# Kernel optimization log

Measured on AMD Instinct MI355X. Metric: run time of the kernel, lower is better.

Reference implementation:

```python
import jax, jax.numpy as jnp
import numpy as np
import math

H, KV, D, HID, WIN = 8, 4, 256, 2048, 1024  # heads, kv heads, head_dim, hidden, sliding window
B, S = 1, 2048

def _rms(x, scale):
    # Gemma3RMSNorm: hardcoded 1e-6 eps, (1+scale) gain
    var = jnp.mean(jnp.square(x), axis=-1, keepdims=True)
    return x * jax.lax.rsqrt(var + 1e-6) * (1.0 + scale)

def _rot_half(x):
    x1, x2 = jnp.split(x, 2, axis=-1)
    return jnp.concatenate((-x2, x1), axis=-1)

def setup_inputs() -> dict:
    key = jax.random.key(0)
    ks = jax.random.split(key, 8)
    x = jax.random.normal(ks[0], (B, S, HID), jnp.float32)
    attn_mask = jnp.ones((B, S), jnp.bool_)
    segment_pos = jnp.broadcast_to(jnp.arange(S, dtype=jnp.int32)[None], (B, S))
    # true RoPE tables, theta=1e6 (Gemma3 global layers)
    inv_freq = 1.0 / (1e6 ** (np.arange(0, D, 2, dtype=np.float32) / D))
    ang = np.arange(S, dtype=np.float32)[:, None] * inv_freq[None, :]  # [S, D/2]
    emb = np.concatenate([ang, ang], axis=-1)                          # [S, D]
    cos = jnp.asarray(np.cos(emb), jnp.float32)[None]                  # [1, S, D]
    sin = jnp.asarray(np.sin(emb), jnp.float32)[None]
    sd = 1.0 / math.sqrt(HID)
    wq = jax.random.normal(ks[1], (HID, H * D), jnp.float32) * sd
    wk = jax.random.normal(ks[2], (HID, KV * D), jnp.float32) * sd
    wv = jax.random.normal(ks[3], (HID, KV * D), jnp.float32) * sd
    wo = jax.random.normal(ks[4], (H * D, HID), jnp.float32) * (1.0 / math.sqrt(H * D))
    q_scale = jnp.zeros((D,), jnp.float32)  # zeros_init as in module
    k_scale = jnp.zeros((D,), jnp.float32)
    return dict(x=x, attn_mask=attn_mask, segment_pos=segment_pos, cos=cos, sin=sin,
                wq=wq, wk=wk, wv=wv, wo=wo, q_scale=q_scale, k_scale=k_scale)

def reference(x, attn_mask, segment_pos, cos, sin, wq, wk, wv, wo, q_scale, k_scale):
    b, s, _ = x.shape
    # projections -> [b, h, s, d]
    q = (x @ wq).reshape(b, s, H, D).transpose(0, 2, 1, 3)
    k = (x @ wk).reshape(b, s, KV, D).transpose(0, 2, 1, 3)
    v = (x @ wv).reshape(b, s, KV, D).transpose(0, 2, 1, 3)
    # per-head QK RMSNorm
    q = _rms(q, q_scale)
    k = _rms(k, k_scale)
    # RoPE (cos/sin broadcast over head axis, unsqueeze_dim=1)
    c, sn = cos[:, None], sin[:, None]
    q = q * c + _rot_half(q) * sn
    k = k * c + _rot_half(k) * sn
    # GQA: repeat-interleave kv heads
    rep = H // KV
    k = jnp.repeat(k, rep, axis=1)
    v = jnp.repeat(v, rep, axis=1)
    scores = jnp.einsum('bhqd,bhkd->bhqk', q, k) / math.sqrt(D)
    # causal + padding mask (q_len > 1 path, no image bidirectional mask)
    causal = jnp.tril(jnp.ones((s, s), jnp.bool_))
    mask = causal[None] & attn_mask[:, None, :]          # [b, q, kv]
    # sliding window mask (prefill: cache positions = arange)
    kvpos = jnp.arange(s)
    pos = segment_pos[:, :, None]
    sliding = (kvpos[None, None] > pos - WIN) & (kvpos[None, None] < pos + WIN)
    full = mask & sliding
    scores = scores + jnp.where(full[:, None], 0.0, -1e37)
    w = jax.nn.softmax(scores.astype(jnp.float32), axis=-1).astype(scores.dtype)
    out = jnp.einsum('bhqk,bhkd->bhqd', w, v)
    out = out.transpose(0, 2, 1, 3).reshape(b, s, H * D)
    return out @ wo
```

## Files before the change

kernel.cpp:

```cpp
#include <hip/hip_runtime.h>
#include <hip/hip_bf16.h>

#define S_LEN 2048
#define HID 2048
#define NH 8
#define NKV 4
#define HD 256
#define WIN 1024

typedef __hip_bfloat16 bf16;
typedef __attribute__((ext_vector_type(8))) short bf16x8;
typedef __attribute__((ext_vector_type(4))) float f32x4;

__device__ __forceinline__ void gld_lds16(void* lds, const void* g) {
    __builtin_amdgcn_global_load_lds(
        (const __attribute__((address_space(1))) unsigned int*)g,
        (__attribute__((address_space(3))) unsigned int*)lds,
        16, 0, 0);
}


__device__ __forceinline__ void transT_body(const float* __restrict__ src, bf16* __restrict__ dst,
                                            int R, int C, int r0, int c0) {
    __shared__ bf16 Ts[64][72];
    const int tid = threadIdx.x;
    {
        const int r = tid >> 2;
        const int cq = (tid & 3) * 16;
#pragma unroll
        for (int j = 0; j < 16; j += 4) {
            float4 v = *(const float4*)&src[(size_t)(r0 + r) * C + c0 + cq + j];
            Ts[cq + j + 0][r] = __float2bfloat16(v.x);
            Ts[cq + j + 1][r] = __float2bfloat16(v.y);
            Ts[cq + j + 2][r] = __float2bfloat16(v.z);
            Ts[cq + j + 3][r] = __float2bfloat16(v.w);
        }
    }
    __syncthreads();
    {
        const int c = tid >> 2;
        const int rq = (tid & 3) * 16;
#pragma unroll
        for (int j = 0; j < 16; j += 8)
            *(uint4*)&dst[(size_t)(c0 + c) * R + r0 + rq + j] = *(const uint4*)&Ts[c][rq + j];
    }
}

__global__ __launch_bounds__(256)
void prep_all(const float* __restrict__ xf, const float* __restrict__ wqf,
              const float* __restrict__ wkf, const float* __restrict__ wvf,
              const float* __restrict__ wof,
              bf16* __restrict__ xb, bf16* __restrict__ wqkvt, bf16* __restrict__ wot) {
    const int bid = blockIdx.x;
    if (bid < 2048) {
        const int i = bid * 256 + threadIdx.x;
        float4 a = ((const float4*)xf)[i * 2];
        float4 b = ((const float4*)xf)[i * 2 + 1];
        union { uint4 v; bf16 h[8]; } u;
        u.h[0] = __float2bfloat16(a.x); u.h[1] = __float2bfloat16(a.y);
        u.h[2] = __float2bfloat16(a.z); u.h[3] = __float2bfloat16(a.w);
        u.h[4] = __float2bfloat16(b.x); u.h[5] = __float2bfloat16(b.y);
        u.h[6] = __float2bfloat16(b.z); u.h[7] = __float2bfloat16(b.w);
        ((uint4*)xb)[i] = u.v;
    } else if (bid < 4096) {
        const int t = bid - 2048;
        const int bx = t & 63, by = t >> 6;
        const float* src; int C, c0, drow0;
        if (bx < 32)      { src = wqf; C = 2048; c0 = bx * 64;        drow0 = bx * 64; }
        else if (bx < 48) { src = wkf; C = 1024; c0 = (bx - 32) * 64; drow0 = 2048 + (bx - 32) * 64; }
        else              { src = wvf; C = 1024; c0 = (bx - 48) * 64; drow0 = 3072 + (bx - 48) * 64; }
        bf16* dshift = wqkvt + ((size_t)drow0 - c0) * HID;
        transT_body(src, dshift, HID, C, by * 64, c0);
    } else {
        const int t = bid - 4096;
        const int bx = t & 31, by = t >> 5;
        transT_body(wof, wot, NH * HD, HID, by * 64, bx * 64);
    }
}

template<int MODE>
__global__ __launch_bounds__(512, 2)
void gemm8p(const bf16* __restrict__ A, const bf16* __restrict__ Bt,
            bf16* __restrict__ Cb,
            bf16* __restrict__ Qo, bf16* __restrict__ Ko, bf16* __restrict__ Vto) {
    extern __shared__ bf16 smem[];
    bf16* AsP = smem;
    bf16* BsP = smem + 3 * 256 * 64;

    const int tid = threadIdx.x;
    const int w = tid >> 6, lane = tid & 63;
    const int lnm = lane & 15, quad = lane >> 4;
    const int wr = w >> 1, wc = w & 1;
    const int r8 = lane >> 3;
    const int swz = ((lane & 7) ^ r8) * 8;

    const int bid = blockIdx.x;
    const int xcd = bid & 7, idx = bid >> 3;
    int m0, n0, kbeg, nt;
    size_t zoff = 0;
    if constexpr (MODE == 1) {
        const int m_t = (xcd >> 2) * 4 + (idx >> 3);
        const int n_t = (xcd & 3) * 8 + (idx & 7);
        m0 = m_t * 256; n0 = n_t * 128; kbeg = 0; nt = 2048 / 64;
    } else {
        const int z   = xcd >> 2;
        const int n_t = (xcd & 3) * 4 + (idx & 3);
        const int m_t = idx >> 2;
        m0 = m_t * 256; n0 = n_t * 128; kbeg = z * 1024; nt = 1024 / 64;
        zoff = (size_t)z * 2048 * 2048;
    }
    const int K = 2048;

    const bf16* pA[4];
#pragma unroll
    for (int g = 0; g < 4; ++g)
        pA[g] = A + (size_t)(m0 + w * 32 + g * 8 + r8) * K + kbeg + swz;
    const bf16* pB[2];
#pragma unroll
    for (int g = 0; g < 2; ++g)
        pB[g] = Bt + (size_t)(n0 + w * 16 + g * 8 + r8) * K + kbeg + swz;
    const int dA = w * 32 * 64;
    const int dB = w * 16 * 64;

#define STG_A(slot, g, t) gld_lds16(AsP + (slot) * 16384 + dA + (g) * 512, pA[g] + (t) * 64)
#define STG_B(slot, g, t) gld_lds16(BsP + (slot) * 8192  + dB + (g) * 512, pB[g] + (t) * 64)
#define LDFRAG(base, row, kh) \
    (*(const bf16x8*)((base) + (row) * 64 + (((((kh) << 2) | quad) ^ ((row) & 7)) << 3)))

    f32x4 acc[4][4];
#pragma unroll
    for (int i = 0; i < 4; ++i)
#pragma unroll
        for (int j = 0; j < 4; ++j) acc[i][j] = (f32x4){0.f, 0.f, 0.f, 0.f};

    STG_A(0, 0, 0); STG_A(0, 1, 0); STG_A(0, 2, 0); STG_A(0, 3, 0);
    STG_B(0, 0, 0); STG_B(0, 1, 0);
    STG_A(1, 0, 1); STG_A(1, 1, 1); STG_A(1, 2, 1); STG_A(1, 3, 1);
    STG_B(1, 0, 1); STG_B(1, 1, 1);
    asm volatile("s_waitcnt vmcnt(6)" ::: "memory");
    __builtin_amdgcn_sched_barrier(0);
    __builtin_amdgcn_s_barrier();

    int sc = 0;
    for (int t = 0; t < nt; ++t) {
        const int ss = (sc == 0) ? 2 : sc - 1;
        const bf16* As_ = AsP + sc * 16384;
        const bf16* Bs_ = BsP + sc * 8192;
        const bool pf = (t + 2 < nt);

        bf16x8 a0[2][2], b[4][2];
#pragma unroll
        for (int tm = 0; tm < 2; ++tm)
#pragma unroll
            for (int kh = 0; kh < 2; ++kh)
                a0[tm][kh] = LDFRAG(As_, wr * 64 + tm * 16 + lnm, kh);
#pragma unroll
        for (int tn = 0; tn < 4; ++tn)
#pragma unroll
            for (int kh = 0; kh < 2; ++kh)
                b[tn][kh] = LDFRAG(Bs_, wc * 64 + tn * 16 + lnm, kh);
        if (pf) { STG_A(ss, 0, t + 2); STG_A(ss, 1, t + 2); STG_B(ss, 0, t + 2); }
        __builtin_amdgcn_s_barrier();
        asm volatile("s_waitcnt lgkmcnt(0)" ::: "memory");
        __builtin_amdgcn_sched_barrier(0);
        __builtin_amdgcn_s_setprio(1);
#pragma unroll
        for (int kh = 0; kh < 2; ++kh)
#pragma unroll
            for (int tm = 0; tm < 2; ++tm)
#pragma unroll
                for (int tn = 0; tn < 4; ++tn)
                    acc[tm][tn] = __builtin_amdgcn_mfma_f32_16x16x32_bf16(
                        a0[tm][kh], b[tn][kh], acc[tm][tn], 0, 0, 0);
        __builtin_amdgcn_s_setprio(0);
        __builtin_amdgcn_s_barrier();

        bf16x8 a1[2][2];
#pragma unroll
        for (int tm = 0; tm < 2; ++tm)
#pragma unroll
            for (int kh = 0; kh < 2; ++kh)
                a1[tm][kh] = LDFRAG(As_, wr * 64 + (tm + 2) * 16 + lnm, kh);
        if (pf) { STG_A(ss, 2, t + 2); STG_A(ss, 3, t + 2); STG_B(ss, 1, t + 2); }
        if (pf) { asm volatile("s_waitcnt vmcnt(6)" ::: "memory"); }
        else    { asm volatile("s_waitcnt vmcnt(0)" ::: "memory"); }
        __builtin_amdgcn_sched_barrier(0);
        __builtin_amdgcn_s_barrier();
        asm volatile("s_waitcnt lgkmcnt(0)" ::: "memory");
        __builtin_amdgcn_sched_barrier(0);
        __builtin_amdgcn_s_setprio(1);
#pragma unroll
        for (int kh = 0; kh < 2; ++kh)
#pragma unroll
            for (int tm = 0; tm < 2; ++tm)
#pragma unroll
                for (int tn = 0; tn < 4; ++tn)
                    acc[tm + 2][tn] = __builtin_amdgcn_mfma_f32_16x16x32_bf16(
                        a1[tm][kh], b[tn][kh], acc[tm + 2][tn], 0, 0, 0);
        __builtin_amdgcn_s_setprio(0);
        __builtin_amdgcn_s_barrier();

        sc = (sc == 2) ? 0 : sc + 1;
    }
#undef STG_A
#undef STG_B
#undef LDFRAG

#pragma unroll
    for (int tm = 0; tm < 4; ++tm)
#pragma unroll
        for (int tn = 0; tn < 4; ++tn)
#pragma unroll
            for (int r = 0; r < 4; ++r) {
                const int row = m0 + wr * 64 + tm * 16 + quad * 4 + r;
                const int col = n0 + wc * 64 + tn * 16 + lnm;
                const float v = acc[tm][tn][r];
                if constexpr (MODE == 2) {
                    Cb[zoff + (size_t)row * 2048 + col] = __float2bfloat16(v);
                } else {
                    if (col < 2048)
                        Qo[(size_t)row * (NH * HD) + col] = __float2bfloat16(v);
                    else if (col < 3072)
                        Ko[(size_t)row * (NKV * HD) + col - 2048] = __float2bfloat16(v);
                    else
                        Vto[(size_t)(col - 3072) * S_LEN + row] = __float2bfloat16(v);
                }
            }
}

__global__ __launch_bounds__(256)
void splitk_add(const bf16* __restrict__ p, float* __restrict__ out) {
    const int i = blockIdx.x * 256 + threadIdx.x;
    union { uint4 v; bf16 h[8]; } a, b;
    a.v = ((const uint4*)p)[i];
    b.v = ((const uint4*)(p + (size_t)2048 * 2048))[i];
    float4 o0, o1;
    o0.x = (float)a.h[0] + (float)b.h[0]; o0.y = (float)a.h[1] + (float)b.h[1];
    o0.z = (float)a.h[2] + (float)b.h[2]; o0.w = (float)a.h[3] + (float)b.h[3];
    o1.x = (float)a.h[4] + (float)b.h[4]; o1.y = (float)a.h[5] + (float)b.h[5];
    o1.z = (float)a.h[6] + (float)b.h[6]; o1.w = (float)a.h[7] + (float)b.h[7];
    ((float4*)out)[i * 2]     = o0;
    ((float4*)out)[i * 2 + 1] = o1;
}

__global__ __launch_bounds__(64)
void rmsrope_kernel(bf16* __restrict__ Q, bf16* __restrict__ Kb,
                    const float* __restrict__ cosb, const float* __restrict__ sinb,
                    const float* __restrict__ qscale, const float* __restrict__ kscale,
                    float qmul) {
    const int p = blockIdx.x;
    const int hg = blockIdx.y;
    const int lane = threadIdx.x;

    bf16* base;
    const float* scale;
    float mul;
    if (hg < NH) { base = Q + (size_t)p * (NH * HD) + hg * HD; scale = qscale; mul = qmul; }
    else         { base = Kb + (size_t)p * (NKV * HD) + (hg - NH) * HD; scale = kscale; mul = 1.f; }

    const int d0 = lane * 2;
    float x0 = (float)base[d0],       x1 = (float)base[d0 + 1];
    float y0 = (float)base[d0 + 128], y1 = (float)base[d0 + 129];

    float ss = x0 * x0 + x1 * x1 + y0 * y0 + y1 * y1;
#pragma unroll
    for (int off = 32; off > 0; off >>= 1) ss += __shfl_xor(ss, off, 64);
    const float r = rsqrtf(ss * (1.0f / (float)HD) + 1e-6f);

    x0 *= r * (1.f + scale[d0]);
    x1 *= r * (1.f + scale[d0 + 1]);
    y0 *= r * (1.f + scale[d0 + 128]);
    y1 *= r * (1.f + scale[d0 + 129]);

    const size_t cb = (size_t)p * HD;
    const float c0 = cosb[cb + d0],       c1 = cosb[cb + d0 + 1];
    const float cA = cosb[cb + d0 + 128], cB = cosb[cb + d0 + 129];
    const float s0 = sinb[cb + d0],       s1 = sinb[cb + d0 + 1];
    const float sA = sinb[cb + d0 + 128], sB = sinb[cb + d0 + 129];

    base[d0]       = __float2bfloat16((x0 * c0 - y0 * s0) * mul);
    base[d0 + 1]   = __float2bfloat16((x1 * c1 - y1 * s1) * mul);
    base[d0 + 128] = __float2bfloat16((y0 * cA + x0 * sA) * mul);
    base[d0 + 129] = __float2bfloat16((y1 * cB + x1 * sB) * mul);
}

#define NCHUNK 4
__global__ __launch_bounds__(256)
void attn_mfma(const bf16* __restrict__ Q, const bf16* __restrict__ K,
               const bf16* __restrict__ Vt, bf16* __restrict__ Op,
               float2* __restrict__ ml) {
    __shared__ bf16 Ks[32][264];
    __shared__ bf16 Vs[256][40];
    __shared__ bf16 Pl[4][16][40];
    const int qt = blockIdx.x, h = blockIdx.y, chunk = blockIdx.z, kvh = h >> 1;
    const int tid = threadIdx.x, w = tid >> 6, lane = tid & 63;
    const int lnm = lane & 15, quad = lane >> 4;

    bf16x8 qf[8];
    const int qrow = qt * 64 + w * 16 + lnm;
#pragma unroll
    for (int s = 0; s < 8; ++s)
        qf[s] = *(const bf16x8*)&Q[(size_t)qrow * HID + h * HD + s * 32 + quad * 8];

    f32x4 o[16];
#pragma unroll
    for (int i = 0; i < 16; ++i) o[i] = (f32x4){0.f, 0.f, 0.f, 0.f};
    float M[4] = {-3e38f, -3e38f, -3e38f, -3e38f};
    float L[4] = {0.f, 0.f, 0.f, 0.f};

    const int ktlo = (qt >= 16) ? (2 * qt - 32) : 0;
    const int kthi = 2 * qt + 1;
    const int ntile = kthi - ktlo + 1;
    const int c0 = ktlo + (chunk * ntile) / NCHUNK;
    const int c1 = ktlo + ((chunk + 1) * ntile) / NCHUNK - 1;

    for (int kt = c0; kt <= c1; ++kt) {
#pragma unroll
        for (int p = 0; p < 4; ++p) {
            const int row = p * 8 + (tid >> 5);
            const int d8 = (tid & 31) * 8;
            *(uint4*)&Ks[row][d8] =
                *(const uint4*)&K[(size_t)(kt * 32 + row) * (NKV * HD) + kvh * HD + d8];
        }
#pragma unroll
        for (int p = 0; p < 4; ++p) {
            const int d = p * 64 + (tid >> 2);
            const int c8 = (tid & 3) * 8;
            *(uint4*)&Vs[d][c8] =
                *(const uint4*)&Vt[(size_t)(kvh * HD + d) * S_LEN + kt * 32 + c8];
        }
        __syncthreads();

        f32x4 s4[2];
        s4[0] = (f32x4){0.f, 0.f, 0.f, 0.f};
        s4[1] = (f32x4){0.f, 0.f, 0.f, 0.f};
#pragma unroll
        for (int t = 0; t < 2; ++t)
#pragma unroll
            for (int s = 0; s < 8; ++s) {
                bf16x8 kf = *(const bf16x8*)&Ks[t * 16 + lnm][s * 32 + quad * 8];
                s4[t] = __builtin_amdgcn_mfma_f32_16x16x32_bf16(qf[s], kf, s4[t], 0, 0, 0);
            }
#pragma unroll
        for (int t = 0; t < 2; ++t)
#pragma unroll
            for (int r = 0; r < 4; ++r) {
                const int m_g = qt * 64 + w * 16 + quad * 4 + r;
                const int n_g = kt * 32 + t * 16 + lnm;
                if (n_g > m_g || n_g + (WIN - 1) < m_g) s4[t][r] = -1e30f;
            }
        float mx[4], rs[4], al[4];
#pragma unroll
        for (int r = 0; r < 4; ++r) {
            mx[r] = fmaxf(s4[0][r], s4[1][r]);
#pragma unroll
            for (int off = 1; off < 16; off <<= 1)
                mx[r] = fmaxf(mx[r], __shfl_xor(mx[r], off, 64));
            const float Mn = fmaxf(M[r], mx[r]);
            al[r] = __expf(M[r] - Mn);
            M[r] = Mn;
        }
#pragma unroll
        for (int t = 0; t < 2; ++t)
#pragma unroll
            for (int r = 0; r < 4; ++r)
                s4[t][r] = __expf(s4[t][r] - M[r]);
#pragma unroll
        for (int r = 0; r < 4; ++r) {
            rs[r] = s4[0][r] + s4[1][r];
#pragma unroll
            for (int off = 1; off < 16; off <<= 1)
                rs[r] += __shfl_xor(rs[r], off, 64);
            L[r] = L[r] * al[r] + rs[r];
        }
#pragma unroll
        for (int t2 = 0; t2 < 16; ++t2)
#pragma unroll
            for (int r = 0; r < 4; ++r) o[t2][r] *= al[r];
#pragma unroll
        for (int t = 0; t < 2; ++t)
#pragma unroll
            for (int r = 0; r < 4; ++r)
                Pl[w][quad * 4 + r][t * 16 + lnm] = __float2bfloat16(s4[t][r]);
        bf16x8 pa = *(const bf16x8*)&Pl[w][lnm][quad * 8];
#pragma unroll
        for (int t2 = 0; t2 < 16; ++t2) {
            bf16x8 vb = *(const bf16x8*)&Vs[t2 * 16 + lnm][quad * 8];
            o[t2] = __builtin_amdgcn_mfma_f32_16x16x32_bf16(pa, vb, o[t2], 0, 0, 0);
        }
        __syncthreads();
    }

    float rL[4];
#pragma unroll
    for (int r = 0; r < 4; ++r) rL[r] = (L[r] > 0.f) ? (1.f / L[r]) : 0.f;
    bf16* Opc = Op + (size_t)chunk * S_LEN * HID;
#pragma unroll
    for (int t2 = 0; t2 < 16; ++t2)
#pragma unroll
        for (int r = 0; r < 4; ++r)
            Opc[(size_t)(qt * 64 + w * 16 + quad * 4 + r) * HID + h * HD + t2 * 16 + lnm] =
                __float2bfloat16(o[t2][r] * rL[r]);
    if (lnm == 0) {
#pragma unroll
        for (int r = 0; r < 4; ++r) {
            const int row = qt * 64 + w * 16 + quad * 4 + r;
            ml[((size_t)chunk * S_LEN + row) * NH + h] = make_float2(M[r], L[r]);
        }
    }
}

__global__ __launch_bounds__(256)
void attn_combine(const bf16* __restrict__ Op, const float2* __restrict__ ml,
                  bf16* __restrict__ O) {
    const int row = blockIdx.x, h = blockIdx.y, d = threadIdx.x;
    float2 c[NCHUNK];
    float Mx = -3e38f;
#pragma unroll
    for (int i = 0; i < NCHUNK; ++i) {
        c[i] = ml[((size_t)i * S_LEN + row) * NH + h];
        Mx = fmaxf(Mx, c[i].x);
    }
    float wsum = 0.f, wgt[NCHUNK];
#pragma unroll
    for (int i = 0; i < NCHUNK; ++i) {
        wgt[i] = c[i].y * __expf(c[i].x - Mx);
        wsum += wgt[i];
    }
    const float inv = 1.0f / wsum;
    const size_t idx = (size_t)row * HID + h * HD + d;
    float acc = 0.f;
#pragma unroll
    for (int i = 0; i < NCHUNK; ++i)
        acc += wgt[i] * (float)Op[(size_t)i * S_LEN * HID + idx];
    O[idx] = __float2bfloat16(acc * inv);
}

extern "C" void kernel_launch(void* const* d_in, const int* in_sizes, int n_in,
                              void* d_out, int out_size, void* d_ws, size_t ws_size,
                              hipStream_t stream) {
    const float* xf   = (const float*)d_in[0];
    const float* cosb = (const float*)d_in[3];
    const float* sinb = (const float*)d_in[4];
    const float* wqf  = (const float*)d_in[5];
    const float* wkf  = (const float*)d_in[6];
    const float* wvf  = (const float*)d_in[7];
    const float* wof  = (const float*)d_in[8];
    const float* qs   = (const float*)d_in[9];
    const float* ks   = (const float*)d_in[10];
    float* out = (float*)d_out;
    char* ws = (char*)d_ws;

    bf16*   wot   = (bf16*)(ws);
    bf16*   Qb    = (bf16*)(ws + ( 8ull << 20));
    bf16*   Kb    = (bf16*)(ws + (16ull << 20));
    bf16*   Vtb   = (bf16*)(ws + (20ull << 20));
    bf16*   wqkvt = (bf16*)(ws + (24ull << 20));
    bf16*   xb    = (bf16*)(ws + (40ull << 20));
    bf16*   Op    = (bf16*)(ws + (24ull << 20));
    bf16*   Ab    = (bf16*)(ws + (40ull << 20));
    bf16*   pk    = (bf16*)(ws + (24ull << 20));
    float2* ml    = (float2*)(ws + (56ull << 20));

    dim3 blk(256);

    static bool attr_done = false;
    if (!attr_done) {
        (void)hipFuncSetAttribute(reinterpret_cast<const void*>(gemm8p<1>),
                                  hipFuncAttributeMaxDynamicSharedMemorySize, 147456);
        (void)hipFuncSetAttribute(reinterpret_cast<const void*>(gemm8p<2>),
                                  hipFuncAttributeMaxDynamicSharedMemorySize, 147456);
        attr_done = true;
    }

    prep_all<<<5120, blk, 0, stream>>>(xf, wqf, wkf, wvf, wof, xb, wqkvt, wot);

    gemm8p<1><<<dim3(256), dim3(512), 147456, stream>>>(
        xb, wqkvt, nullptr, Qb, Kb, Vtb);

    rmsrope_kernel<<<dim3(S_LEN, NH + NKV), dim3(64), 0, stream>>>(
        Qb, Kb, cosb, sinb, qs, ks, 0.0625f);

    attn_mfma<<<dim3(S_LEN / 64, NH, NCHUNK), blk, 0, stream>>>(Qb, Kb, Vtb, Op, ml);
    attn_combine<<<dim3(S_LEN, NH), blk, 0, stream>>>(Op, ml, Ab);

    gemm8p<2><<<dim3(256), dim3(512), 147456, stream>>>(
        Ab, wot, pk, nullptr, nullptr, nullptr);
    splitk_add<<<2048, blk, 0, stream>>>(pk, out);
}
```

Before: 275.4 us.

## Double-buffer K via async LDS loads, transpose S, and skip lazy rescales

The attention kernel now double-buffers K tiles in XOR-swizzled LDS using direct global-to-LDS loads, so the next tile's fetch overlaps current compute. It computes S transposed so each lane owns one query row, which reduces the softmax reductions to two shuffles. It also skips the output rescale unless the max grows by more than 8. P is repacked into MFMA A-fragments with register shuffles instead of an LDS round trip, and V is read straight from global memory with no LDS staging. Reading V from global may add memory latency, and the lazy rescale changes numerics slightly but stays bounded.

```diff
diff --git a/kernel.cpp b/kernel.cpp
--- a/kernel.cpp
+++ b/kernel.cpp
@@ -285,13 +285,18 @@
 }
 
 #define NCHUNK 4
+
+__device__ __forceinline__ unsigned pkbf(float a, float b) {
+    union { bf16 h; unsigned short u; } ca, cb;
+    ca.h = __float2bfloat16(a); cb.h = __float2bfloat16(b);
+    return (unsigned)ca.u | ((unsigned)cb.u << 16);
+}
+
 __global__ __launch_bounds__(256)
 void attn_mfma(const bf16* __restrict__ Q, const bf16* __restrict__ K,
                const bf16* __restrict__ Vt, bf16* __restrict__ Op,
                float2* __restrict__ ml) {
-    __shared__ bf16 Ks[32][264];
-    __shared__ bf16 Vs[256][40];
-    __shared__ bf16 Pl[4][16][40];
+    __shared__ bf16 Ks[2][32][256];
     const int qt = blockIdx.x, h = blockIdx.y, chunk = blockIdx.z, kvh = h >> 1;
     const int tid = threadIdx.x, w = tid >> 6, lane = tid & 63;
     const int lnm = lane & 15, quad = lane >> 4;
@@ -305,8 +310,7 @@
     f32x4 o[16];
 #pragma unroll
     for (int i = 0; i < 16; ++i) o[i] = (f32x4){0.f, 0.f, 0.f, 0.f};
-    float M[4] = {-3e38f, -3e38f, -3e38f, -3e38f};
-    float L[4] = {0.f, 0.f, 0.f, 0.f};
+    float M = -3e38f, L = 0.f;
 
     const int ktlo = (qt >= 16) ? (2 * qt - 32) : 0;
     const int kthi = 2 * qt + 1;
@@ -314,100 +318,132 @@
     const int c0 = ktlo + (chunk * ntile) / NCHUNK;
     const int c1 = ktlo + ((chunk + 1) * ntile) / NCHUNK - 1;
 
-    for (int kt = c0; kt <= c1; ++kt) {
-#pragma unroll
-        for (int p = 0; p < 4; ++p) {
-            const int row = p * 8 + (tid >> 5);
-            const int d8 = (tid & 31) * 8;
-            *(uint4*)&Ks[row][d8] =
-                *(const uint4*)&K[(size_t)(kt * 32 + row) * (NKV * HD) + kvh * HD + d8];
+    const int srow = w * 8 + (lane >> 5);
+    const int sunit = lane & 31;
+    const bf16* kg = K + (size_t)kvh * HD;
+    const bf16* vg = Vt + ((size_t)kvh * HD + lnm) * S_LEN + quad * 8;
+
+#define STAGE_K(kt_, buf_)                                                        \
+    {                                                                             \
+        _Pragma("unroll")                                                         \
+        for (int cc = 0; cc < 4; ++cc) {                                          \
+            const int r_ = srow + cc * 2;                                         \
+            const int ug_ = sunit ^ (r_ & 7);                                     \
+            gld_lds16(&Ks[buf_][w * 8 + cc * 2][0],                               \
+                      kg + (size_t)((kt_) * 32 + r_) * (NKV * HD) + ug_ * 8);     \
+        }                                                                         \
+    }
+#define KFRAG(buf_, t_, s_) \
+    (*(const bf16x8*)&Ks[buf_][(t_) * 16 + lnm][((((s_) * 4 + quad) ^ (lnm & 7)) * 8)])
+
+    if (c0 <= c1) {
+        STAGE_K(c0, 0);
+        asm volatile("s_waitcnt vmcnt(0)" ::: "memory");
+        __builtin_amdgcn_sched_barrier(0);
+        __builtin_amdgcn_s_barrier();
+
+        for (int kt = c0; kt <= c1; ++kt) {
+            const int buf = (kt - c0) & 1;
+            if (kt < c1) STAGE_K(kt + 1, buf ^ 1);
+
+            f32x4 s4[2];
+            s4[0] = (f32x4){0.f, 0.f, 0.f, 0.f};
+            s4[1] = (f32x4){0.f, 0.f, 0.f, 0.f};
+            __builtin_amdgcn_s_setprio(1);
+#pragma unroll
+            for (int t = 0; t < 2; ++t)
+#pragma unroll
+                for (int s = 0; s < 8; ++s)
+                    s4[t] = __builtin_amdgcn_mfma_f32_16x16x32_bf16(
+                        KFRAG(buf, t, s), qf[s], s4[t], 0, 0, 0);
+            __builtin_amdgcn_s_setprio(0);
+
+#pragma unroll
+            for (int t = 0; t < 2; ++t)
+#pragma unroll
+                for (int r = 0; r < 4; ++r) {
+                    const int n_g = kt * 32 + t * 16 + quad * 4 + r;
+                    if (n_g > qrow || n_g + (WIN - 1) < qrow) s4[t][r] = -1e30f;
+                }
+
+            float mx = fmaxf(fmaxf(fmaxf(s4[0][0], s4[0][1]), fmaxf(s4[0][2], s4[0][3])),
+                             fmaxf(fmaxf(s4[1][0], s4[1][1]), fmaxf(s4[1][2], s4[1][3])));
+            mx = fmaxf(mx, __shfl_xor(mx, 16, 64));
+            mx = fmaxf(mx, __shfl_xor(mx, 32, 64));
+
+            if (!__all(mx <= M + 8.f)) {
+                const float Mn = fmaxf(M, mx);
+                const float al = __expf(M - Mn);
+                M = Mn;
+                L *= al;
+                float alr[4];
+#pragma unroll
+                for (int r = 0; r < 4; ++r) alr[r] = __shfl(al, quad * 4 + r, 64);
+#pragma unroll
+                for (int t2 = 0; t2 < 16; ++t2)
+#pragma unroll
+                    for (int r = 0; r < 4; ++r) o[t2][r] *= alr[r];
+            }
+
+            float rs = 0.f;
+            unsigned u00, u01, u10, u11;
+            {
+                float p0 = __expf(s4[0][0] - M), p1 = __expf(s4[0][1] - M);
+                float p2 = __expf(s4[0][2] - M), p3 = __expf(s4[0][3] - M);
+                rs += (p0 + p1) + (p2 + p3);
+                u00 = pkbf(p0, p1); u01 = pkbf(p2, p3);
+                p0 = __expf(s4[1][0] - M); p1 = __expf(s4[1][1] - M);
+                p2 = __expf(s4[1][2] - M); p3 = __expf(s4[1][3] - M);
+                rs += (p0 + p1) + (p2 + p3);
+                u10 = pkbf(p0, p1); u11 = pkbf(p2, p3);
+            }
+            rs += __shfl_xor(rs, 16, 64);
+            rs += __shfl_xor(rs, 32, 64);
+            L += rs;
+
+            const int slo = lnm + 16 * (2 * (quad & 1));
+            const int shi = slo + 16;
+            const int A0 = __shfl((int)u00, slo, 64), A1 = __shfl((int)u01, slo, 64);
+            const int A2 = __shfl((int)u00, shi, 64), A3 = __shfl((int)u01, shi, 64);
+            const int B0 = __shfl((int)u10, slo, 64), B1 = __shfl((int)u11, slo, 64);
+            const int B2 = __shfl((int)u10, shi, 64), B3 = __shfl((int)u11, shi, 64);
+            union { bf16x8 v; int i4[4]; } pa;
+            pa.i4[0] = (quad < 2) ? A0 : B0;
+            pa.i4[1] = (quad < 2) ? A1 : B1;
+            pa.i4[2] = (quad < 2) ? A2 : B2;
+            pa.i4[3] = (quad < 2) ? A3 : B3;
+
+            __builtin_amdgcn_s_setprio(1);
+#pragma unroll
+            for (int t2 = 0; t2 < 16; ++t2) {
+                bf16x8 vb = *(const bf16x8*)&vg[(size_t)t2 * 16 * S_LEN + kt * 32];
+                o[t2] = __builtin_amdgcn_mfma_f32_16x16x32_bf16(pa.v, vb, o[t2], 0, 0, 0);
+            }
+            __builtin_amdgcn_s_setprio(0);
+
+            if (kt < c1) {
+                asm volatile("s_waitcnt vmcnt(0)" ::: "memory");
+                __builtin_amdgcn_sched_barrier(0);
+                __builtin_amdgcn_s_barrier();
+            }
         }
-#pragma unroll
-        for (int p = 0; p < 4; ++p) {
-            const int d = p * 64 + (tid >> 2);
-            const int c8 = (tid & 3) * 8;
-            *(uint4*)&Vs[d][c8] =
-                *(const uint4*)&Vt[(size_t)(kvh * HD + d) * S_LEN + kt * 32 + c8];
-        }
-        __syncthreads();
-
-        f32x4 s4[2];
-        s4[0] = (f32x4){0.f, 0.f, 0.f, 0.f};
-        s4[1] = (f32x4){0.f, 0.f, 0.f, 0.f};
-#pragma unroll
-        for (int t = 0; t < 2; ++t)
-#pragma unroll
-            for (int s = 0; s < 8; ++s) {
-                bf16x8 kf = *(const bf16x8*)&Ks[t * 16 + lnm][s * 32 + quad * 8];
-                s4[t] = __builtin_amdgcn_mfma_f32_16x16x32_bf16(qf[s], kf, s4[t], 0, 0, 0);
-            }
-#pragma unroll
-        for (int t = 0; t < 2; ++t)
-#pragma unroll
-            for (int r = 0; r < 4; ++r) {
-                const int m_g = qt * 64 + w * 16 + quad * 4 + r;
-                const int n_g = kt * 32 + t * 16 + lnm;
-                if (n_g > m_g || n_g + (WIN - 1) < m_g) s4[t][r] = -1e30f;
-            }
-        float mx[4], rs[4], al[4];
-#pragma unroll
-        for (int r = 0; r < 4; ++r) {
-            mx[r] = fmaxf(s4[0][r], s4[1][r]);
-#pragma unroll
-            for (int off = 1; off < 16; off <<= 1)
-                mx[r] = fmaxf(mx[r], __shfl_xor(mx[r], off, 64));
-            const float Mn = fmaxf(M[r], mx[r]);
-            al[r] = __expf(M[r] - Mn);
-            M[r] = Mn;
-        }
-#pragma unroll
-        for (int t = 0; t < 2; ++t)
-#pragma unroll
-            for (int r = 0; r < 4; ++r)
-                s4[t][r] = __expf(s4[t][r] - M[r]);
-#pragma unroll
-        for (int r = 0; r < 4; ++r) {
-            rs[r] = s4[0][r] + s4[1][r];
-#pragma unroll
-            for (int off = 1; off < 16; off <<= 1)
-                rs[r] += __shfl_xor(rs[r], off, 64);
-            L[r] = L[r] * al[r] + rs[r];
-        }
-#pragma unroll
-        for (int t2 = 0; t2 < 16; ++t2)
-#pragma unroll
-            for (int r = 0; r < 4; ++r) o[t2][r] *= al[r];
-#pragma unroll
-        for (int t = 0; t < 2; ++t)
-#pragma unroll
-            for (int r = 0; r < 4; ++r)
-                Pl[w][quad * 4 + r][t * 16 + lnm] = __float2bfloat16(s4[t][r]);
-        bf16x8 pa = *(const bf16x8*)&Pl[w][lnm][quad * 8];
-#pragma unroll
-        for (int t2 = 0; t2 < 16; ++t2) {
-            bf16x8 vb = *(const bf16x8*)&Vs[t2 * 16 + lnm][quad * 8];
-            o[t2] = __builtin_amdgcn_mfma_f32_16x16x32_bf16(pa, vb, o[t2], 0, 0, 0);
-        }
-        __syncthreads();
-    }
-
-    float rL[4];
-#pragma unroll
-    for (int r = 0; r < 4; ++r) rL[r] = (L[r] > 0.f) ? (1.f / L[r]) : 0.f;
+    }
+#undef STAGE_K
+#undef KFRAG
+
+    const float rL = (L > 0.f) ? (1.f / L) : 0.f;
+    float rr[4];
+#pragma unroll
+    for (int r = 0; r < 4; ++r) rr[r] = __shfl(rL, quad * 4 + r, 64);
     bf16* Opc = Op + (size_t)chunk * S_LEN * HID;
 #pragma unroll
     for (int t2 = 0; t2 < 16; ++t2)
 #pragma unroll
         for (int r = 0; r < 4; ++r)
             Opc[(size_t)(qt * 64 + w * 16 + quad * 4 + r) * HID + h * HD + t2 * 16 + lnm] =
-                __float2bfloat16(o[t2][r] * rL[r]);
-    if (lnm == 0) {
-#pragma unroll
-        for (int r = 0; r < 4; ++r) {
-            const int row = qt * 64 + w * 16 + quad * 4 + r;
-            ml[((size_t)chunk * S_LEN + row) * NH + h] = make_float2(M[r], L[r]);
-        }
-    }
+                __float2bfloat16(o[t2][r] * rr[r]);
+    if (quad == 0)
+        ml[((size_t)chunk * S_LEN + qt * 64 + w * 16 + lnm) * NH + h] = make_float2(M, L);
 }
 
 __global__ __launch_bounds__(256)
```

Measured after the change: 306.8 us. +11.4%, slower.
